# Kernel tuning notes

Measured on AMD Instinct MI355X. Metric: run time of the kernel, lower is better.

The kernel has to match this reference:

```python
import jax, jax.numpy as jnp
import numpy as np

E = 6          # num_experts
TOP_K = 2
FUT = 60       # future_len
DIM = 128

def _gelu(x):
    return jax.nn.gelu(x, approximate=False)  # torch nn.GELU default is exact erf


def setup_inputs() -> dict:
    key = jax.random.key(0)
    ks = jax.random.split(key, 20)
    B, M, D = 8192, 6, DIM
    s = 0.02
    inp = {
        "mode_features": jax.random.normal(ks[0], (B, M, D), jnp.float32),
        # router MLP: D->256->128->E  (dropout is identity in eval mode)
        "rW1": jax.random.normal(ks[1], (D, 256)) * s, "rb1": jnp.zeros((256,)),
        "rW2": jax.random.normal(ks[2], (256, 128)) * s, "rb2": jnp.zeros((128,)),
        "rW3": jax.random.normal(ks[3], (128, E)) * s, "rb3": jnp.zeros((E,)),
        # stacked expert trajectory heads: D->256->256->2*FUT
        "tW1": jax.random.normal(ks[4], (E, D, 256)) * s, "tb1": jnp.zeros((E, 256)),
        "tW2": jax.random.normal(ks[5], (E, 256, 256)) * s, "tb2": jnp.zeros((E, 256)),
        "tW3": jax.random.normal(ks[6], (E, 256, 2 * FUT)) * s, "tb3": jnp.zeros((E, 2 * FUT)),
        # stacked expert score heads: D->128->64->1
        "sW1": jax.random.normal(ks[7], (E, D, 128)) * s, "sb1": jnp.zeros((E, 128)),
        "sW2": jax.random.normal(ks[8], (E, 128, 64)) * s, "sb2": jnp.zeros((E, 64)),
        "sW3": jax.random.normal(ks[9], (E, 64, 1)) * s, "sb3": jnp.zeros((E, 1)),
    }
    return {k: v.astype(jnp.float32) for k, v in inp.items()}


def reference(mode_features, rW1, rb1, rW2, rb2, rW3, rb3,
              tW1, tb1, tW2, tb2, tW3, tb3,
              sW1, sb1, sW2, sb2, sW3, sb3):
    B, M, D = mode_features.shape
    x = mode_features.reshape(B * M, D)  # [N, D]

    # ---- router (dropout = identity at inference) ----
    h = _gelu(x @ rW1 + rb1)
    h = _gelu(h @ rW2 + rb2)
    logits = h @ rW3 + rb3                      # [N, E]
    router_probs = jax.nn.softmax(logits, axis=-1)

    top_v, top_i = jax.lax.top_k(logits, TOP_K)  # [N, K]
    top_w = jax.nn.softmax(top_v, axis=-1)       # renormalized top-k weights

    # ---- all experts, dense over E (then gather top-k) ----
    th = _gelu(jnp.einsum('nd,edh->neh', x, tW1) + tb1)   # [N, E, 256]
    th = _gelu(jnp.einsum('neh,ehg->neg', th, tW2) + tb2) # [N, E, 256]
    traj_all = jnp.einsum('neh,eho->neo', th, tW3) + tb3  # [N, E, 2*FUT]

    sh = _gelu(jnp.einsum('nd,edh->neh', x, sW1) + sb1)   # [N, E, 128]
    sh = _gelu(jnp.einsum('neh,ehg->neg', sh, sW2) + sb2) # [N, E, 64]
    score_all = (jnp.einsum('neh,eho->neo', sh, sW3) + sb3)[..., 0]  # [N, E]

    traj_sel = jnp.take_along_axis(traj_all, top_i[:, :, None], axis=1)  # [N, K, 2*FUT]
    score_sel = jnp.take_along_axis(score_all, top_i, axis=1)            # [N, K]

    trajectories = (top_w[:, :, None] * traj_sel).sum(axis=1).reshape(B, M, FUT, 2)
    scores = (top_w * score_sel).sum(axis=1).reshape(B, M)

    # ---- load-balance aux loss ----
    avg_probs = router_probs.mean(axis=0)  # [E]
    entropy = -(avg_probs * jnp.log(avg_probs + 1e-8)).sum()
    lb_loss = -entropy * 0.01
    l2_loss = jnp.mean((avg_probs - 1.0 / E) ** 2)
    aux_loss = lb_loss + 0.01 * l2_loss

    return trajectories, scores, aux_loss, router_probs.reshape(B, M, E)
```

## Files before the change

kernel.cpp:

```cpp
#include <hip/hip_runtime.h>

#define N_TOK 49152
#define PER_E 155648
#define NSTAGE 19
#define RSTAGES 24
#define MAXTILES 774

#define TRAJ_OFF 0
#define SCORE_OFF 5898240
#define AUX_OFF  5947392
#define PROB_OFF 5947393

typedef __attribute__((ext_vector_type(8))) short short8v;
typedef __attribute__((ext_vector_type(4))) float f32x4;
typedef __attribute__((ext_vector_type(4))) unsigned short u16x4;

typedef __attribute__((address_space(3))) unsigned char lds_byte;
typedef __attribute__((address_space(1))) const unsigned char gl_byte;

__device__ __forceinline__ unsigned short f2bf(float f) {
  unsigned int u = __float_as_uint(f);
  u = (u + 0x7FFFu + ((u >> 16) & 1u)) >> 16;
  return (unsigned short)u;
}
__device__ __forceinline__ float bf2f(unsigned short h) {
  return __uint_as_float(((unsigned int)h) << 16);
}
__device__ __forceinline__ unsigned int pkbf(float a, float b) {
  unsigned int r;
  asm("v_cvt_pk_bf16_f32 %0, %1, %2" : "=v"(r) : "v"(a), "v"(b));
  return r;
}
__device__ __forceinline__ float geluf(float v) {
  float x = v * 0.70710678118654752f;
  float ax = fabsf(x);
  float t = __builtin_amdgcn_rcpf(fmaf(0.3275911f, ax, 1.0f));
  float p = t * fmaf(t, fmaf(t, fmaf(t, fmaf(t, 1.061405429f, -1.453152027f),
                                     1.421413741f), -0.284496736f), 0.254829592f);
  float er = 1.0f - p * __expf(-ax * ax);
  er = copysignf(er, x);
  return 0.5f * v * (1.0f + er);
}
__device__ __forceinline__ float geluf_fast(float v) {
  float x = v * 0.70710678f;
  float ax = fabsf(x);
  float t = __builtin_amdgcn_rcpf(fmaf(0.47047f, ax, 1.0f));
  float poly = t * fmaf(t, fmaf(t, 0.7478556f, -0.0958798f), 0.3480242f);
  float er = fmaf(-poly, __expf(-ax * ax), 1.0f);
  er = copysignf(er, x);
  return 0.5f * v * (1.0f + er);
}

__global__ __launch_bounds__(256) void prep_weights(
    const float* __restrict__ tW1, const float* __restrict__ tW2, const float* __restrict__ tW3,
    const float* __restrict__ sW1, const float* __restrict__ sW2,
    unsigned short* __restrict__ blob)
{
  int id = blockIdx.x * 256 + threadIdx.x;
  if (id >= 6 * PER_E) return;
  int e = id / PER_E;
  int r = id - e * PER_E;
  int p = r >> 13;
  int q = r & 8191;
  int f = q >> 9;
  int l = (q >> 3) & 63;
  int j = q & 7;
  int hi = l >> 4, rl = l & 15;
  const float* src; int N, tile, ks; bool perm;
  if (p < 2)       { src = sW1 + e * 16384; N = 128; tile = 4 * p + (f >> 2);        ks = f & 3; perm = false; }
  else if (p == 2) { src = sW2 + e * 8192;  N = 64;  tile = f >> 2;                  ks = f & 3; perm = true;  }
  else if (p < 7)  { src = tW1 + e * 32768; N = 256; tile = 4 * (p - 3) + (f >> 2);  ks = f & 3; perm = false; }
  else if (p < 11) { src = tW2 + e * 65536; N = 256; tile = 2 * (p - 7) + (f >> 3);  ks = f & 7; perm = true;  }
  else if (p < 13) { src = tW3 + e * 30720; N = 120; tile = f >> 1;  ks = 2 * (p - 11) + (f & 1); perm = true; }
  else if (p < 17) { src = tW2 + e * 65536; N = 256; tile = 8 + 2 * (p - 13) + (f >> 3); ks = f & 7; perm = true; }
  else             { src = tW3 + e * 30720; N = 120; tile = f >> 1;  ks = 4 + 2 * (p - 17) + (f & 1); perm = true; }
  int k = ks * 32 + (perm ? (16 * (j >> 2) + 4 * hi + (j & 3)) : (8 * hi + j));
  int unit = tile * 16 + rl;
  blob[id] = f2bf(unit < N ? src[k * N + unit] : 0.0f);
}

__global__ __launch_bounds__(256) void prep_router(
    const float* __restrict__ rW1, const float* __restrict__ rW2,
    unsigned short* __restrict__ rblob)
{
  int id = blockIdx.x * 256 + threadIdx.x;
  if (id >= RSTAGES * 8192) return;
  int p = id >> 13;
  int q = id & 8191;
  int f = q >> 9;
  int l = (q >> 3) & 63;
  int j = q & 7;
  int hi = l >> 4, rl = l & 15;
  const float* src; int N, tile, ks, part; bool perm;
  if (p < 12) { int c = p / 3; part = p % 3; src = rW1; N = 256; tile = 4 * c + (f >> 2); ks = f & 3; perm = false; }
  else        { int c = (p - 12) / 3; part = (p - 12) % 3; src = rW2; N = 128; tile = 2 * c + (f >> 3); ks = f & 7; perm = true; }
  int k = ks * 32 + (perm ? (16 * (j >> 2) + 4 * hi + (j & 3)) : (8 * hi + j));
  int unit = tile * 16 + rl;
  float v = (unit < N) ? src[k * N + unit] : 0.0f;
  unsigned short b0 = f2bf(v);
  float r1 = v - bf2f(b0);
  unsigned short b1 = f2bf(r1);
  float r2 = r1 - bf2f(b1);
  unsigned short b2 = f2bf(r2);
  rblob[id] = (part == 0) ? b0 : ((part == 1) ? b1 : b2);
}

__device__ __forceinline__ f32x4 MM16(short8v a, short8v b, f32x4 c) {
  return __builtin_amdgcn_mfma_f32_16x16x32_bf16(a, b, c, 0, 0, 0);
}
__device__ __forceinline__ void cvt16(f32x4 aE, f32x4 aO, const float* bp, int hi, short8v& fr) {
  float g[8];
  #pragma unroll
  for (int j = 0; j < 8; ++j) {
    float v = (j < 4) ? aE[j & 3] : aO[j & 3];
    int unit = 16 * (j >> 2) + 4 * hi + (j & 3);
    g[j] = geluf_fast(v + bp[unit]);
  }
  unsigned int* pr = (unsigned int*)&fr;
  pr[0] = pkbf(g[0], g[1]); pr[1] = pkbf(g[2], g[3]);
  pr[2] = pkbf(g[4], g[5]); pr[3] = pkbf(g[6], g[7]);
}
__device__ __forceinline__ void cvt16s(f32x4 aE, f32x4 aO, const float* bp, int hi,
                                       short8v& f0, short8v& f1) {
  #pragma unroll
  for (int j = 0; j < 8; ++j) {
    float v = (j < 4) ? aE[j & 3] : aO[j & 3];
    int unit = 16 * (j >> 2) + 4 * hi + (j & 3);
    float g = geluf(v + bp[unit]);
    unsigned short b0 = f2bf(g);
    f0[j] = (short)b0;
    f1[j] = (short)f2bf(g - bf2f(b0));
  }
}

#define FRAG(s, f) (*(const short8v*)(&wlds[((s) % 3) * 8192 + (f) * 512 + lane * 8]))

#define RSTAGE(s) do { \
    const unsigned short* gsrc_ = rblob + (s) * 8192 + w * 1024 + lane * 8; \
    unsigned short* ldst_ = &wlds[((s) % 3) * 8192 + w * 1024]; \
    _Pragma("unroll") \
    for (int i_ = 0; i_ < 2; ++i_) \
      __builtin_amdgcn_global_load_lds((gl_byte*)(gsrc_ + i_ * 512), (lds_byte*)(ldst_ + i_ * 512), 16, 0, 0); \
  } while (0)

#define RPIPE(s, nw) do { \
    asm volatile("s_waitcnt vmcnt(" #nw ")" ::: "memory"); \
    __builtin_amdgcn_sched_barrier(0); \
    __builtin_amdgcn_s_barrier(); \
    __builtin_amdgcn_sched_barrier(0); \
    if ((s) + 2 < RSTAGES) RSTAGE((s) + 2); \
  } while (0)

__global__ __launch_bounds__(512, 4) void router_mfma(
    const float* __restrict__ x, const unsigned short* __restrict__ rblob,
    const float* __restrict__ rb1, const float* __restrict__ rb2,
    const float* __restrict__ rW3, const float* __restrict__ rb3,
    float* __restrict__ probs_out,
    int* __restrict__ pairTok, float* __restrict__ pairW, int* __restrict__ pairIdx,
    int* __restrict__ cnt, float* __restrict__ probsum)
{
  __shared__ __align__(16) unsigned short wlds[3 * 8192];
  __shared__ float bLds[1160];
  __shared__ float probsLds[768];
  __shared__ float psum[8];
  __shared__ int lcnt[8], gbase[8];

  int tid = threadIdx.x;
  int lane = tid & 63;
  int w = tid >> 6;
  int col = lane & 15;
  int hi = lane >> 4;
  int tok0 = blockIdx.x * 128;
  int myTok = tok0 + w * 16 + col;

  if (tid < 256) bLds[tid] = rb1[tid];
  else if (tid < 384) bLds[tid] = rb2[tid - 256];
  for (int i = tid; i < 768; i += 512) bLds[384 + i] = rW3[i];
  if (tid < 6) bLds[1152 + tid] = rb3[tid];
  if (tid < 8) { psum[tid] = 0.f; lcnt[tid] = 0; }

  short8v xf0[4], xf1[4], xf2[4];
  {
    const float* px = x + (size_t)myTok * 128 + hi * 8;
    #pragma unroll
    for (int ks = 0; ks < 4; ++ks) {
      f32x4 lo = *(const f32x4*)(px + ks * 32);
      f32x4 hv = *(const f32x4*)(px + ks * 32 + 4);
      #pragma unroll
      for (int j = 0; j < 8; ++j) {
        float v = (j < 4) ? lo[j & 3] : hv[j & 3];
        unsigned short b0 = f2bf(v);
        float r1 = v - bf2f(b0);
        unsigned short b1 = f2bf(r1);
        float r2 = r1 - bf2f(b1);
        xf0[ks][j] = (short)b0;
        xf1[ks][j] = (short)b1;
        xf2[ks][j] = (short)f2bf(r2);
      }
    }
  }
  __syncthreads();

  RSTAGE(0);
  RSTAGE(1);

  short8v h0B[8], h1B[8];
  #pragma unroll
  for (int c = 0; c < 4; ++c) {
    f32x4 acc[4] = {};
    RPIPE(3 * c, 2);
    #pragma unroll
    for (int ks = 0; ks < 4; ++ks)
      #pragma unroll
      for (int u = 0; u < 4; ++u) {
        short8v wf = FRAG(3 * c, u * 4 + ks);
        acc[u] = MM16(wf, xf0[ks], acc[u]);
        acc[u] = MM16(wf, xf1[ks], acc[u]);
        acc[u] = MM16(wf, xf2[ks], acc[u]);
      }
    RPIPE(3 * c + 1, 2);
    #pragma unroll
    for (int ks = 0; ks < 4; ++ks)
      #pragma unroll
      for (int u = 0; u < 4; ++u) {
        short8v wf = FRAG(3 * c + 1, u * 4 + ks);
        acc[u] = MM16(wf, xf0[ks], acc[u]);
        acc[u] = MM16(wf, xf1[ks], acc[u]);
      }
    RPIPE(3 * c + 2, 2);
    #pragma unroll
    for (int ks = 0; ks < 4; ++ks)
      #pragma unroll
      for (int u = 0; u < 4; ++u) {
        short8v wf = FRAG(3 * c + 2, u * 4 + ks);
        acc[u] = MM16(wf, xf0[ks], acc[u]);
      }
    cvt16s(acc[0], acc[1], bLds + 32 * (2 * c),     hi, h0B[2 * c],     h1B[2 * c]);
    cvt16s(acc[2], acc[3], bLds + 32 * (2 * c + 1), hi, h0B[2 * c + 1], h1B[2 * c + 1]);
  }

  f32x4 acc2[8] = {};
  #pragma unroll
  for (int d = 0; d < 4; ++d) {
    RPIPE(12 + 3 * d, 2);
    #pragma unroll
    for (int ks = 0; ks < 8; ++ks)
      #pragma unroll
      for (int u = 0; u < 2; ++u) {
        short8v wf = FRAG(12 + 3 * d, u * 8 + ks);
        int t = 2 * d + u;
        acc2[t] = MM16(wf, h0B[ks], acc2[t]);
        acc2[t] = MM16(wf, h1B[ks], acc2[t]);
      }
    RPIPE(12 + 3 * d + 1, 2);
    #pragma unroll
    for (int ks = 0; ks < 8; ++ks)
      #pragma unroll
      for (int u = 0; u < 2; ++u) {
        short8v wf = FRAG(12 + 3 * d + 1, u * 8 + ks);
        int t = 2 * d + u;
        acc2[t] = MM16(wf, h0B[ks], acc2[t]);
        acc2[t] = MM16(wf, h1B[ks], acc2[t]);
      }
    if (d < 3) { RPIPE(12 + 3 * d + 2, 2); }
    else       { RPIPE(23, 0); }
    #pragma unroll
    for (int ks = 0; ks < 8; ++ks)
      #pragma unroll
      for (int u = 0; u < 2; ++u) {
        short8v wf = FRAG(12 + 3 * d + 2, u * 8 + ks);
        int t = 2 * d + u;
        acc2[t] = MM16(wf, h0B[ks], acc2[t]);
      }
  }

  float pl[6] = {0.f, 0.f, 0.f, 0.f, 0.f, 0.f};
  #pragma unroll
  for (int t = 0; t < 8; ++t)
    #pragma unroll
    for (int r = 0; r < 4; ++r) {
      int unit = t * 16 + 4 * hi + r;
      float h2 = geluf(acc2[t][r] + bLds[256 + unit]);
      #pragma unroll
      for (int e = 0; e < 6; ++e)
        pl[e] = fmaf(h2, bLds[384 + unit * 6 + e], pl[e]);
    }
  #pragma unroll
  for (int e = 0; e < 6; ++e) {
    pl[e] += __shfl_xor(pl[e], 16);
    pl[e] += __shfl_xor(pl[e], 32);
  }

  int i1 = 0, i2 = 0, lp1 = 0, lp2 = 0;
  float ww1 = 0.f, ww2 = 0.f;
  if (hi == 0) {
    float l0[6];
    #pragma unroll
    for (int e = 0; e < 6; ++e) l0[e] = pl[e] + bLds[1152 + e];
    float m = l0[0];
    #pragma unroll
    for (int e = 1; e < 6; ++e) m = fmaxf(m, l0[e]);
    float pe[6]; float ssum = 0.f;
    #pragma unroll
    for (int e = 0; e < 6; ++e) { pe[e] = expf(l0[e] - m); ssum += pe[e]; }
    float inv = 1.f / ssum;
    int lrow = w * 16 + col;
    #pragma unroll
    for (int e = 0; e < 6; ++e) {
      float prb = pe[e] * inv;
      probsLds[lrow * 6 + e] = prb;
      atomicAdd(&psum[e], prb);
    }
    float v1 = l0[0]; i1 = 0; float v2 = -1e30f; i2 = -1;
    #pragma unroll
    for (int e = 1; e < 6; ++e) {
      float v = l0[e];
      if (v > v1) { v2 = v1; i2 = i1; v1 = v; i1 = e; }
      else if (v > v2) { v2 = v; i2 = e; }
    }
    float e2 = expf(v2 - v1);
    float den = 1.f / (1.f + e2);
    ww1 = den; ww2 = e2 * den;
    lp1 = atomicAdd(&lcnt[i1], 1);
    lp2 = atomicAdd(&lcnt[i2], 1);
  }
  __syncthreads();
  if (tid < 6) gbase[tid] = atomicAdd(&cnt[tid], lcnt[tid]);
  __syncthreads();
  if (hi == 0) {
    int g1 = gbase[i1] + lp1, g2 = gbase[i2] + lp2;
    pairTok[i1 * N_TOK + g1] = myTok; pairW[i1 * N_TOK + g1] = ww1;
    pairTok[i2 * N_TOK + g2] = myTok; pairW[i2 * N_TOK + g2] = ww2;
    pairIdx[2 * myTok]     = i1 * N_TOK + g1;
    pairIdx[2 * myTok + 1] = i2 * N_TOK + g2;
  }
  if (tid < 6) atomicAdd(&probsum[tid], psum[tid]);
  for (int i = tid; i < 768; i += 512)
    probs_out[(size_t)tok0 * 6 + i] = probsLds[i];
}

__global__ void aux_kernel(const float* __restrict__ probsum, const int* __restrict__ cnt,
                           int* __restrict__ csum, int* __restrict__ ntiles, int* __restrict__ tiles,
                           float* __restrict__ auxout)
{
  if (threadIdx.x == 0 && blockIdx.x == 0) {
    int s = 0;
    for (int e = 0; e < 6; ++e) { csum[e] = s; s += cnt[e]; }
    int nt = 0;
    for (int e = 0; e < 6; ++e)
      for (int b = 0; b < cnt[e]; b += 128)
        tiles[nt++] = (e << 16) | (b >> 7);
    ntiles[0] = nt;
    float ent = 0.f, l2 = 0.f;
    for (int e = 0; e < 6; ++e) {
      float avg = probsum[e] / (float)N_TOK;
      ent -= avg * logf(avg + 1e-8f);
      float d = avg - (1.0f / 6.0f);
      l2 += d * d;
    }
    l2 *= (1.0f / 6.0f);
    auxout[0] = -ent * 0.01f + 0.01f * l2;
  }
}

#define STAGE(s) do { \
    const unsigned short* gsrc_ = eblob + (s) * 8192 + w * 1024 + lane * 8; \
    unsigned short* ldst_ = &wlds[((s) % 3) * 8192 + w * 1024]; \
    _Pragma("unroll") \
    for (int i_ = 0; i_ < 2; ++i_) \
      __builtin_amdgcn_global_load_lds((gl_byte*)(gsrc_ + i_ * 512), (lds_byte*)(ldst_ + i_ * 512), 16, 0, 0); \
  } while (0)

#define PIPE(s, nw) do { \
    asm volatile("s_waitcnt vmcnt(" #nw ")" ::: "memory"); \
    __builtin_amdgcn_sched_barrier(0); \
    __builtin_amdgcn_s_barrier(); \
    __builtin_amdgcn_sched_barrier(0); \
    if ((s) + 2 < NSTAGE) STAGE((s) + 2); \
  } while (0)

template<int OUTMODE>
__global__ __launch_bounds__(512, 4) void expert_kernel(
    const float* __restrict__ x,
    const unsigned short* __restrict__ blob,
    const float* __restrict__ tb1, const float* __restrict__ tb2, const float* __restrict__ tb3,
    const float* __restrict__ sb1, const float* __restrict__ sb2,
    const float* __restrict__ sW3, const float* __restrict__ sb3,
    const int* __restrict__ pairTok, const float* __restrict__ pairW,
    const int* __restrict__ cnt, const int* __restrict__ csum,
    const int* __restrict__ ntiles, const int* __restrict__ tiles,
    float* __restrict__ traj_out, float* __restrict__ score_out,
    unsigned short* __restrict__ trajP, float* __restrict__ scoreP)
{
  if (blockIdx.x >= (unsigned)ntiles[0]) return;
  int ent = tiles[blockIdx.x];
  int e = ent >> 16;
  int base = (ent & 0xffff) << 7;
  int count = cnt[e];

  __shared__ __align__(16) unsigned short wlds[3 * 8192];
  __shared__ float bLds[896];
  __shared__ int   toksLds[128];
  __shared__ float gwsLds[128];

  int tid = threadIdx.x;
  int lane = tid & 63;
  int w = tid >> 6;
  int col = lane & 15;
  int hi = lane >> 4;
  const unsigned short* eblob = blob + (size_t)e * PER_E;
  int slotbase = csum[e] + base;

  if (tid < 128) {
    int idx = e * N_TOK + base + ((base + tid < count) ? tid : 0);
    toksLds[tid] = pairTok[idx];
    gwsLds[tid] = (base + tid < count) ? pairW[idx] : 0.f;
  }
  if (tid < 128) bLds[tid] = sb1[e * 128 + tid];
  if (tid < 64)  bLds[128 + tid] = sb2[e * 64 + tid];
  if (tid < 64)  bLds[192 + tid] = sW3[e * 64 + tid];
  if (tid < 256) { bLds[256 + tid] = tb1[e * 256 + tid]; bLds[512 + tid] = tb2[e * 256 + tid]; }
  if (tid < 120) bLds[768 + tid] = tb3[e * 120 + tid];
  __syncthreads();

  int row = w * 16 + col;
  int tok = toksLds[row];
  bool valid = (base + row < count);
  float gw = gwsLds[row];

  short8v xf[4];
  {
    const float* px = x + (size_t)tok * 128 + hi * 8;
    #pragma unroll
    for (int ks = 0; ks < 4; ++ks) {
      f32x4 lo = *(const f32x4*)(px + ks * 32);
      f32x4 hv = *(const f32x4*)(px + ks * 32 + 4);
      unsigned int* pt = (unsigned int*)&xf[ks];
      pt[0] = pkbf(lo[0], lo[1]); pt[1] = pkbf(lo[2], lo[3]);
      pt[2] = pkbf(hv[0], hv[1]); pt[3] = pkbf(hv[2], hv[3]);
    }
  }

  STAGE(0);
  STAGE(1);

  short8v sB[4];
  {
    f32x4 a[4] = {};
    PIPE(0, 2);
    #pragma unroll
    for (int f = 0; f < 16; ++f)
      a[f >> 2] = MM16(FRAG(0, f), xf[f & 3], a[f >> 2]);
    cvt16(a[0], a[1], bLds + 0,  hi, sB[0]);  cvt16(a[2], a[3], bLds + 32, hi, sB[1]);
    f32x4 b[4] = {};
    PIPE(1, 2);
    #pragma unroll
    for (int f = 0; f < 16; ++f)
      b[f >> 2] = MM16(FRAG(1, f), xf[f & 3], b[f >> 2]);
    cvt16(b[0], b[1], bLds + 64, hi, sB[2]);  cvt16(b[2], b[3], bLds + 96, hi, sB[3]);
  }

  float p0 = 0.f;
  {
    f32x4 q[4] = {};
    PIPE(2, 2);
    #pragma unroll
    for (int f = 0; f < 16; ++f)
      q[f >> 2] = MM16(FRAG(2, f), sB[f & 3], q[f >> 2]);
    #pragma unroll
    for (int t = 0; t < 4; ++t)
      #pragma unroll
      for (int r = 0; r < 4; ++r) {
        int unit = t * 16 + 4 * hi + r;
        p0 += geluf_fast(q[t][r] + bLds[128 + unit]) * bLds[192 + unit];
      }
    p0 += __shfl_xor(p0, 16); p0 += __shfl_xor(p0, 32);
  }

  short8v h1B[8];
  #define T1S(t, S) { \
    f32x4 a[4] = {}; \
    PIPE(S, 2); \
    _Pragma("unroll") \
    for (int f = 0; f < 16; ++f) \
      a[f >> 2] = MM16(FRAG(S, f), xf[f & 3], a[f >> 2]); \
    cvt16(a[0], a[1], bLds + 256 + (t) * 64,      hi, h1B[2 * (t)]); \
    cvt16(a[2], a[3], bLds + 256 + (t) * 64 + 32, hi, h1B[2 * (t) + 1]); \
  }
  T1S(0, 3) T1S(1, 4) T1S(2, 5) T1S(3, 6)

  short8v h2B[4];
  #define T2S(s, S, BOFF) { \
    f32x4 u[2] = {}; \
    PIPE(S, 2); \
    _Pragma("unroll") \
    for (int f = 0; f < 16; ++f) \
      u[f >> 3] = MM16(FRAG(S, f), h1B[f & 7], u[f >> 3]); \
    cvt16(u[0], u[1], bLds + 512 + (BOFF) + 32 * (s), hi, h2B[s]); \
  }

  f32x4 wacc[8] = {};
  #define T3S(s, S, NW) { \
    PIPE(S, NW); \
    _Pragma("unroll") \
    for (int f = 0; f < 16; ++f) \
      wacc[f >> 1] = MM16(FRAG(S, f), h2B[2 * (s) + (f & 1)], wacc[f >> 1]); \
  }

  T2S(0, 7, 0) T2S(1, 8, 0) T2S(2, 9, 0) T2S(3, 10, 0)
  T3S(0, 11, 2) T3S(1, 12, 2)
  T2S(0, 13, 128) T2S(1, 14, 128) T2S(2, 15, 128) T2S(3, 16, 128)
  T3S(0, 17, 2) T3S(1, 18, 0)

  if (hi == 0 && valid) {
    float v = gw * (p0 + sb3[e]);
    if (OUTMODE == 0) scoreP[slotbase + row] = v; else atomicAdd(&score_out[tok], v);
  }
  if (valid) {
    if (OUTMODE == 0) {
      unsigned short* dst = trajP + (size_t)(slotbase + row) * 120;
      #pragma unroll
      for (int t = 0; t < 8; ++t)
        #pragma unroll
        for (int r = 0; r < 4; r += 2) {
          int unit = t * 16 + 4 * hi + r;
          if (unit + 1 < 120) {
            float a0 = gw * (wacc[t][r] + bLds[768 + unit]);
            float a1 = gw * (wacc[t][r + 1] + bLds[768 + unit + 1]);
            *(unsigned int*)(dst + unit) = pkbf(a0, a1);
          }
        }
    } else {
      float* dst = traj_out + (size_t)tok * 120;
      #pragma unroll
      for (int t = 0; t < 8; ++t)
        #pragma unroll
        for (int r = 0; r < 4; ++r) {
          int unit = t * 16 + 4 * hi + r;
          if (unit < 120) atomicAdd(&dst[unit], gw * (wacc[t][r] + bLds[768 + unit]));
        }
    }
  }
}

__global__ __launch_bounds__(256) void combine_kernel(
    const int* __restrict__ pairIdx, const int* __restrict__ csum,
    const unsigned short* __restrict__ trajP, const float* __restrict__ scoreP,
    float* __restrict__ traj_out, float* __restrict__ score_out)
{
  int t = blockIdx.x * 256 + threadIdx.x;
  if (t >= N_TOK) return;
  int p0 = pairIdx[2 * t], p1 = pairIdx[2 * t + 1];
  int e0 = p0 / N_TOK, e1 = p1 / N_TOK;
  size_t s0 = (size_t)csum[e0] + (p0 - e0 * N_TOK);
  size_t s1 = (size_t)csum[e1] + (p1 - e1 * N_TOK);
  const unsigned short* r0 = trajP + s0 * 120;
  const unsigned short* r1 = trajP + s1 * 120;
  float* o = traj_out + (size_t)t * 120;
  #pragma unroll 6
  for (int i = 0; i < 30; ++i) {
    u16x4 a = *(const u16x4*)(r0 + i * 4);
    u16x4 b = *(const u16x4*)(r1 + i * 4);
    f32x4 v;
    #pragma unroll
    for (int jj = 0; jj < 4; ++jj) v[jj] = bf2f(a[jj]) + bf2f(b[jj]);
    *(f32x4*)(o + i * 4) = v;
  }
  score_out[t] = scoreP[s0] + scoreP[s1];
}

extern "C" void kernel_launch(void* const* d_in, const int* in_sizes, int n_in,
                              void* d_out, int out_size, void* d_ws, size_t ws_size,
                              hipStream_t stream) {
  (void)in_sizes; (void)n_in; (void)out_size;
  const float* x   = (const float*)d_in[0];
  const float* rW1 = (const float*)d_in[1];
  const float* rb1 = (const float*)d_in[2];
  const float* rW2 = (const float*)d_in[3];
  const float* rb2 = (const float*)d_in[4];
  const float* rW3 = (const float*)d_in[5];
  const float* rb3 = (const float*)d_in[6];
  const float* tW1 = (const float*)d_in[7];
  const float* tb1 = (const float*)d_in[8];
  const float* tW2 = (const float*)d_in[9];
  const float* tb2 = (const float*)d_in[10];
  const float* tW3 = (const float*)d_in[11];
  const float* tb3 = (const float*)d_in[12];
  const float* sW1 = (const float*)d_in[13];
  const float* sb1 = (const float*)d_in[14];
  const float* sW2 = (const float*)d_in[15];
  const float* sb2 = (const float*)d_in[16];
  const float* sW3 = (const float*)d_in[17];
  const float* sb3 = (const float*)d_in[18];
  float* out = (float*)d_out;

  char* wsb = (char*)d_ws;
  int*   cnt     = (int*)(wsb + 0);
  float* probsum = (float*)(wsb + 32);
  int*   csum    = (int*)(wsb + 64);
  int*   ntiles  = (int*)(wsb + 96);
  int*   tiles   = (int*)(wsb + 112);
  const size_t B = 112 + 4 * ((MAXTILES + 7) & ~7);
  int*   pairTok = (int*)(wsb + B);
  float* pairW   = (float*)(wsb + B + (size_t)6 * N_TOK * 4);
  int*   pairIdx = (int*)(wsb + B + (size_t)12 * N_TOK * 4);
  float* scoreP  = (float*)(wsb + B + (size_t)14 * N_TOK * 4);
  unsigned short* blob  = (unsigned short*)(wsb + B + (size_t)16 * N_TOK * 4);
  unsigned short* rblob = (unsigned short*)(wsb + B + (size_t)16 * N_TOK * 4 + (size_t)6 * PER_E * 2);
  unsigned short* trajP = (unsigned short*)(wsb + B + (size_t)16 * N_TOK * 4 + (size_t)6 * PER_E * 2
                                            + (size_t)RSTAGES * 8192 * 2);
  size_t need = B + (size_t)16 * N_TOK * 4 + (size_t)6 * PER_E * 2 + (size_t)RSTAGES * 8192 * 2
              + (size_t)2 * N_TOK * 120 * 2;
  bool scratch = ws_size >= need;

  hipMemsetAsync(wsb, 0, 112, stream);
  if (!scratch) hipMemsetAsync(d_out, 0, (size_t)(N_TOK * 121) * 4, stream);

  prep_weights<<<(6 * PER_E) / 256, 256, 0, stream>>>(tW1, tW2, tW3, sW1, sW2, blob);
  prep_router<<<(RSTAGES * 8192) / 256, 256, 0, stream>>>(rW1, rW2, rblob);
  router_mfma<<<N_TOK / 128, 512, 0, stream>>>(x, rblob, rb1, rb2, rW3, rb3,
                                               out + PROB_OFF, pairTok, pairW, pairIdx, cnt, probsum);
  aux_kernel<<<1, 64, 0, stream>>>(probsum, cnt, csum, ntiles, tiles, out + AUX_OFF);
  if (scratch) {
    expert_kernel<0><<<MAXTILES, 512, 0, stream>>>(
        x, blob, tb1, tb2, tb3, sb1, sb2, sW3, sb3, pairTok, pairW, cnt, csum, ntiles, tiles,
        out + TRAJ_OFF, out + SCORE_OFF, trajP, scoreP);
    combine_kernel<<<N_TOK / 256, 256, 0, stream>>>(pairIdx, csum, trajP, scoreP,
                                                    out + TRAJ_OFF, out + SCORE_OFF);
  } else {
    expert_kernel<1><<<MAXTILES, 512, 0, stream>>>(
        x, blob, tb1, tb2, tb3, sb1, sb2, sW3, sb3, pairTok, pairW, cnt, csum, ntiles, tiles,
        out + TRAJ_OFF, out + SCORE_OFF, trajP, scoreP);
  }
}
```

Baseline: 178.8 us.

## Switch expert kernel to double-buffered weight staging and raise occupancy bound

Measured after the change: 197.7 us. 10.6% more time.

```diff
diff --git a/kernel.cpp b/kernel.cpp
--- a/kernel.cpp
+++ b/kernel.cpp
@@ -133,7 +133,7 @@
   }
 }
 
-#define FRAG(s, f) (*(const short8v*)(&wlds[((s) % 3) * 8192 + (f) * 512 + lane * 8]))
+#define RFRAG(s, f) (*(const short8v*)(&wlds[((s) % 3) * 8192 + (f) * 512 + lane * 8]))
 
 #define RSTAGE(s) do { \
     const unsigned short* gsrc_ = rblob + (s) * 8192 + w * 1024 + lane * 8; \
@@ -213,7 +213,7 @@
     for (int ks = 0; ks < 4; ++ks)
       #pragma unroll
       for (int u = 0; u < 4; ++u) {
-        short8v wf = FRAG(3 * c, u * 4 + ks);
+        short8v wf = RFRAG(3 * c, u * 4 + ks);
         acc[u] = MM16(wf, xf0[ks], acc[u]);
         acc[u] = MM16(wf, xf1[ks], acc[u]);
         acc[u] = MM16(wf, xf2[ks], acc[u]);
@@ -223,7 +223,7 @@
     for (int ks = 0; ks < 4; ++ks)
       #pragma unroll
       for (int u = 0; u < 4; ++u) {
-        short8v wf = FRAG(3 * c + 1, u * 4 + ks);
+        short8v wf = RFRAG(3 * c + 1, u * 4 + ks);
         acc[u] = MM16(wf, xf0[ks], acc[u]);
         acc[u] = MM16(wf, xf1[ks], acc[u]);
       }
@@ -232,7 +232,7 @@
     for (int ks = 0; ks < 4; ++ks)
       #pragma unroll
       for (int u = 0; u < 4; ++u) {
-        short8v wf = FRAG(3 * c + 2, u * 4 + ks);
+        short8v wf = RFRAG(3 * c + 2, u * 4 + ks);
         acc[u] = MM16(wf, xf0[ks], acc[u]);
       }
     cvt16s(acc[0], acc[1], bLds + 32 * (2 * c),     hi, h0B[2 * c],     h1B[2 * c]);
@@ -247,7 +247,7 @@
     for (int ks = 0; ks < 8; ++ks)
       #pragma unroll
       for (int u = 0; u < 2; ++u) {
-        short8v wf = FRAG(12 + 3 * d, u * 8 + ks);
+        short8v wf = RFRAG(12 + 3 * d, u * 8 + ks);
         int t = 2 * d + u;
         acc2[t] = MM16(wf, h0B[ks], acc2[t]);
         acc2[t] = MM16(wf, h1B[ks], acc2[t]);
@@ -257,7 +257,7 @@
     for (int ks = 0; ks < 8; ++ks)
       #pragma unroll
       for (int u = 0; u < 2; ++u) {
-        short8v wf = FRAG(12 + 3 * d + 1, u * 8 + ks);
+        short8v wf = RFRAG(12 + 3 * d + 1, u * 8 + ks);
         int t = 2 * d + u;
         acc2[t] = MM16(wf, h0B[ks], acc2[t]);
         acc2[t] = MM16(wf, h1B[ks], acc2[t]);
@@ -268,7 +268,7 @@
     for (int ks = 0; ks < 8; ++ks)
       #pragma unroll
       for (int u = 0; u < 2; ++u) {
-        short8v wf = FRAG(12 + 3 * d + 2, u * 8 + ks);
+        short8v wf = RFRAG(12 + 3 * d + 2, u * 8 + ks);
         int t = 2 * d + u;
         acc2[t] = MM16(wf, h0B[ks], acc2[t]);
       }
@@ -363,24 +363,26 @@
   }
 }
 
-#define STAGE(s) do { \
+#define EFRAG(s, f) (*(const short8v*)(&wlds[((s) & 1) * 8192 + (f) * 512 + lane * 8]))
+
+#define ESTAGE(s) do { \
     const unsigned short* gsrc_ = eblob + (s) * 8192 + w * 1024 + lane * 8; \
-    unsigned short* ldst_ = &wlds[((s) % 3) * 8192 + w * 1024]; \
+    unsigned short* ldst_ = &wlds[((s) & 1) * 8192 + w * 1024]; \
     _Pragma("unroll") \
     for (int i_ = 0; i_ < 2; ++i_) \
       __builtin_amdgcn_global_load_lds((gl_byte*)(gsrc_ + i_ * 512), (lds_byte*)(ldst_ + i_ * 512), 16, 0, 0); \
   } while (0)
 
-#define PIPE(s, nw) do { \
-    asm volatile("s_waitcnt vmcnt(" #nw ")" ::: "memory"); \
+#define EPIPE(s) do { \
+    asm volatile("s_waitcnt vmcnt(0)" ::: "memory"); \
     __builtin_amdgcn_sched_barrier(0); \
     __builtin_amdgcn_s_barrier(); \
     __builtin_amdgcn_sched_barrier(0); \
-    if ((s) + 2 < NSTAGE) STAGE((s) + 2); \
+    if ((s) + 1 < NSTAGE) ESTAGE((s) + 1); \
   } while (0)
 
 template<int OUTMODE>
-__global__ __launch_bounds__(512, 4) void expert_kernel(
+__global__ __launch_bounds__(512, 8) void expert_kernel(
     const float* __restrict__ x,
     const unsigned short* __restrict__ blob,
     const float* __restrict__ tb1, const float* __restrict__ tb2, const float* __restrict__ tb3,
@@ -398,7 +400,7 @@
   int base = (ent & 0xffff) << 7;
   int count = cnt[e];
 
-  __shared__ __align__(16) unsigned short wlds[3 * 8192];
+  __shared__ __align__(16) unsigned short wlds[2 * 8192];
   __shared__ float bLds[896];
   __shared__ int   toksLds[128];
   __shared__ float gwsLds[128];
@@ -441,32 +443,31 @@
     }
   }
 
-  STAGE(0);
-  STAGE(1);
+  ESTAGE(0);
 
   short8v sB[4];
   {
     f32x4 a[4] = {};
-    PIPE(0, 2);
+    EPIPE(0);
     #pragma unroll
     for (int f = 0; f < 16; ++f)
-      a[f >> 2] = MM16(FRAG(0, f), xf[f & 3], a[f >> 2]);
+      a[f >> 2] = MM16(EFRAG(0, f), xf[f & 3], a[f >> 2]);
     cvt16(a[0], a[1], bLds + 0,  hi, sB[0]);  cvt16(a[2], a[3], bLds + 32, hi, sB[1]);
     f32x4 b[4] = {};
-    PIPE(1, 2);
+    EPIPE(1);
     #pragma unroll
     for (int f = 0; f < 16; ++f)
-      b[f >> 2] = MM16(FRAG(1, f), xf[f & 3], b[f >> 2]);
+      b[f >> 2] = MM16(EFRAG(1, f), xf[f & 3], b[f >> 2]);
     cvt16(b[0], b[1], bLds + 64, hi, sB[2]);  cvt16(b[2], b[3], bLds + 96, hi, sB[3]);
   }
 
   float p0 = 0.f;
   {
     f32x4 q[4] = {};
-    PIPE(2, 2);
+    EPIPE(2);
     #pragma unroll
     for (int f = 0; f < 16; ++f)
-      q[f >> 2] = MM16(FRAG(2, f), sB[f & 3], q[f >> 2]);
+      q[f >> 2] = MM16(EFRAG(2, f), sB[f & 3], q[f >> 2]);
     #pragma unroll
     for (int t = 0; t < 4; ++t)
       #pragma unroll
@@ -480,10 +481,10 @@
   short8v h1B[8];
   #define T1S(t, S) { \
     f32x4 a[4] = {}; \
-    PIPE(S, 2); \
+    EPIPE(S); \
     _Pragma("unroll") \
     for (int f = 0; f < 16; ++f) \
-      a[f >> 2] = MM16(FRAG(S, f), xf[f & 3], a[f >> 2]); \
+      a[f >> 2] = MM16(EFRAG(S, f), xf[f & 3], a[f >> 2]); \
     cvt16(a[0], a[1], bLds + 256 + (t) * 64,      hi, h1B[2 * (t)]); \
     cvt16(a[2], a[3], bLds + 256 + (t) * 64 + 32, hi, h1B[2 * (t) + 1]); \
   }
@@ -492,25 +493,25 @@
   short8v h2B[4];
   #define T2S(s, S, BOFF) { \
     f32x4 u[2] = {}; \
-    PIPE(S, 2); \
+    EPIPE(S); \
     _Pragma("unroll") \
     for (int f = 0; f < 16; ++f) \
-      u[f >> 3] = MM16(FRAG(S, f), h1B[f & 7], u[f >> 3]); \
+      u[f >> 3] = MM16(EFRAG(S, f), h1B[f & 7], u[f >> 3]); \
     cvt16(u[0], u[1], bLds + 512 + (BOFF) + 32 * (s), hi, h2B[s]); \
   }
 
   f32x4 wacc[8] = {};
-  #define T3S(s, S, NW) { \
-    PIPE(S, NW); \
+  #define T3S(s, S) { \
+    EPIPE(S); \
     _Pragma("unroll") \
     for (int f = 0; f < 16; ++f) \
-      wacc[f >> 1] = MM16(FRAG(S, f), h2B[2 * (s) + (f & 1)], wacc[f >> 1]); \
+      wacc[f >> 1] = MM16(EFRAG(S, f), h2B[2 * (s) + (f & 1)], wacc[f >> 1]); \
   }
 
   T2S(0, 7, 0) T2S(1, 8, 0) T2S(2, 9, 0) T2S(3, 10, 0)
-  T3S(0, 11, 2) T3S(1, 12, 2)
+  T3S(0, 11) T3S(1, 12)
   T2S(0, 13, 128) T2S(1, 14, 128) T2S(2, 15, 128) T2S(3, 16, 128)
-  T3S(0, 17, 2) T3S(1, 18, 0)
+  T3S(0, 17) T3S(1, 18)
 
   if (hi == 0 && valid) {
     float v = gw * (p0 + sb3[e]);
```
